# Kernel optimization log

Measured on AMD Instinct MI355X. Metric: run time of the kernel, lower is better.

The kernel has to match this reference:

```python
import jax, jax.numpy as jnp
import numpy as np

C = 32          # mid_channel / in_channel
B = 8           # batch size (number of scenes)
N = 2_000_000   # total points across batch
BN_EPS = 1e-4   # BatchNorm1d eps from norm_fn


def setup_inputs() -> dict:
    key = jax.random.key(0)
    ks = jax.random.split(key, 8)
    s = 0.05
    return {
        "feats": jax.random.normal(ks[0], (N, C), dtype=jnp.float32),
        "batch_idxs": jnp.sort(jax.random.randint(ks[1], (N,), 0, B, dtype=jnp.int32)),
        "off_w1": jax.random.normal(ks[2], (C, C), dtype=jnp.float32) * s,
        "off_b1": jnp.zeros((C,), jnp.float32),
        "bn_gamma": jnp.ones((C,), jnp.float32),   # set_bn_init fills 1.0
        "bn_beta": jnp.zeros((C,), jnp.float32),   # set_bn_init fills 0.0
        "off_w2": jax.random.normal(ks[3], (C, 3), dtype=jnp.float32) * s,
        "off_b2": jnp.zeros((3,), jnp.float32),
        "mask_w1": jax.random.normal(ks[4], (C, C), dtype=jnp.float32) * s,
        "mask_b1": jnp.zeros((C,), jnp.float32),
        "mask_w2": jax.random.normal(ks[5], (C, 1), dtype=jnp.float32) * s,
        "mask_b2": jnp.zeros((1,), jnp.float32),
        "iou_w": jax.random.normal(ks[6], (C, 1), dtype=jnp.float32) * s,
        "iou_b": jnp.zeros((1,), jnp.float32),
    }


def reference(feats, batch_idxs, off_w1, off_b1, bn_gamma, bn_beta, off_w2, off_b2,
              mask_w1, mask_b1, mask_w2, mask_b2, iou_w, iou_b):
    # offset_linear = MLP([C, C, 3], norm_fn=BatchNorm1d): Linear -> BN -> ReLU -> Linear
    h = feats @ off_w1 + off_b1                      # [N, C]
    mu = h.mean(axis=0)
    var = jnp.mean(jnp.square(h - mu), axis=0)       # biased var (torch BN training fwd)
    h = (h - mu) * jax.lax.rsqrt(var + BN_EPS) * bn_gamma + bn_beta
    h = jax.nn.relu(h)
    pt_offsets = h @ off_w2 + off_b2                 # [N, 3]

    # mask_linear = MLP([C, C, 1], norm_fn=None): Linear -> ReLU -> Linear
    m = jax.nn.relu(feats @ mask_w1 + mask_b1)       # [N, C]
    mask_scores = m @ mask_w2 + mask_b2              # [N, 1]

    # global_pool: scatter mean of features over per-batch segments (batch offsets)
    ones = jnp.ones((feats.shape[0],), feats.dtype)
    counts = jax.ops.segment_sum(ones, batch_idxs, num_segments=B)          # [B]
    pooled = jax.ops.segment_sum(feats, batch_idxs, num_segments=B)         # [B, C]
    pooled = pooled / jnp.maximum(counts, 1.0)[:, None]

    # iou_score_linear on the pooled proposal feature
    iou_scores = pooled @ iou_w + iou_b              # [B, 1]
    return pt_offsets, mask_scores, pooled, iou_scores
```

## Files before the change

kernel.cpp:

```cpp
#include <hip/hip_runtime.h>

#define TPB 256
#define GRID1 1024
#define GRID2 1024
#define MSLICES 8

typedef __attribute__((ext_vector_type(8))) short short8;
typedef __attribute__((ext_vector_type(4))) float floatx4;

__device__ __forceinline__ unsigned short bf_trunc(float f){
    union { float f; unsigned u; } c; c.f = f;
    return (unsigned short)(c.u >> 16);
}
__device__ __forceinline__ unsigned short bf_rne(float f){
    union { float f; unsigned u; } c; c.f = f;
    unsigned r = c.u + 0x7fffu + ((c.u >> 16) & 1u);
    return (unsigned short)(r >> 16);
}
__device__ __forceinline__ unsigned pack_bf(float lo, float hi){
    union { float f; unsigned u; } a, b; a.f = lo; b.f = hi;
    return __builtin_amdgcn_perm(b.u, a.u, 0x07060302u);
}
__device__ __forceinline__ float bfbits(unsigned short u){
    union { unsigned u; float f; } c; c.u = ((unsigned)u) << 16; return c.f;
}

__global__ void lb_kernel(const int* __restrict__ bidx, int* __restrict__ ws_lb,
                          int N, int B)
{
    const int t = threadIdx.x;
    if (t <= B){
        int lo = 0, hi = N;
        while (lo < hi){
            const int mid = (lo + hi) >> 1;
            if (bidx[mid] < t) lo = mid + 1; else hi = mid;
        }
        ws_lb[t] = lo;
    }
}

__global__ __launch_bounds__(TPB) void pass1_kernel(
    const float* __restrict__ feats, const int* __restrict__ ws_lb,
    float* __restrict__ ws_pool, float* __restrict__ ws_M,
    int N, int B)
{
    __shared__ float s_stage[TPB/64][1024];
    __shared__ float s_pool[8][32];
    __shared__ float s_M[3][256];
    __shared__ int   s_lb[9];

    const int tid  = threadIdx.x;
    const int lane = tid & 63;
    const int wv   = tid >> 6;
    const int p = lane & 15;
    const int q = lane >> 4;

    ((float*)s_pool)[tid] = 0.f;
    for (int i = tid; i < 768; i += TPB) ((float*)s_M)[i] = 0.f;
    if (tid <= B) s_lb[tid] = ws_lb[tid];
    __syncthreads();

    float pacc[4] = {0,0,0,0};
    floatx4 acc00 = {0,0,0,0}, acc01 = {0,0,0,0}, acc11 = {0,0,0,0};

    const int ngroups = (N + 31) >> 5;
    const int nw  = gridDim.x * (TPB / 64);
    const int wid = blockIdx.x * (TPB / 64) + wv;
    const int g0  = (int)((long)wid       * ngroups / nw);
    const int gE  = (int)((long)(wid + 1) * ngroups / nw);

    int curb = 0;
    { const int r = g0 << 5; while (curb < B - 1 && r >= s_lb[curb + 1]) curb++; }
    int lbn = s_lb[curb + 1];

    float* sw = &s_stage[wv][0];
    const int wrow  = lane >> 3;
    const int wg    = (lane & 7) ^ wrow;
    const int cbase = (lane & 7) << 2;
    const int wo0 = ( 0 + wrow) * 32 + (wg << 2);
    const int wo1 = ( 8 + wrow) * 32 + (wg << 2);
    const int wo2 = (16 + wrow) * 32 + (wg << 2);
    const int wo3 = (24 + wrow) * 32 + (wg << 2);

    floatx4 sv0 = {0,0,0,0}, sv1 = {0,0,0,0}, sv2 = {0,0,0,0}, sv3 = {0,0,0,0};
    if (g0 < gE){
        const float* gp = feats + ((size_t)g0 << 10) + (lane << 2);
        const int r = (g0 << 5) + wrow;
        if (r + 24 < N){
            sv0 = *(const floatx4*)(gp);
            sv1 = *(const floatx4*)(gp + 256);
            sv2 = *(const floatx4*)(gp + 512);
            sv3 = *(const floatx4*)(gp + 768);
        } else {
            if (r      < N) sv0 = *(const floatx4*)(gp);
            if (r +  8 < N) sv1 = *(const floatx4*)(gp + 256);
            if (r + 16 < N) sv2 = *(const floatx4*)(gp + 512);
            if (r + 24 < N) sv3 = *(const floatx4*)(gp + 768);
        }
    }

    for (int g = g0; g < gE; ++g){
        *(floatx4*)(sw + wo0) = sv0;
        *(floatx4*)(sw + wo1) = sv1;
        *(floatx4*)(sw + wo2) = sv2;
        *(floatx4*)(sw + wo3) = sv3;

        floatx4 nv0 = {0,0,0,0}, nv1 = {0,0,0,0}, nv2 = {0,0,0,0}, nv3 = {0,0,0,0};
        if (g + 1 < gE){
            const float* gp = feats + ((size_t)(g + 1) << 10) + (lane << 2);
            const int r = ((g + 1) << 5) + wrow;
            if (r + 24 < N){
                nv0 = *(const floatx4*)(gp);
                nv1 = *(const floatx4*)(gp + 256);
                nv2 = *(const floatx4*)(gp + 512);
                nv3 = *(const floatx4*)(gp + 768);
            } else {
                if (r      < N) nv0 = *(const floatx4*)(gp);
                if (r +  8 < N) nv1 = *(const floatx4*)(gp + 256);
                if (r + 16 < N) nv2 = *(const floatx4*)(gp + 512);
                if (r + 24 < N) nv3 = *(const floatx4*)(gp + 768);
            }
        }

        const int r0 = g << 5;
        if (r0 >= lbn){
#pragma unroll
            for (int j = 0; j < 4; ++j){
                if (pacc[j] != 0.f) atomicAdd(&s_pool[curb][cbase + j], pacc[j]);
                pacc[j] = 0.f;
            }
            do { curb++; } while (curb < B - 1 && r0 >= s_lb[curb + 1]);
            lbn = s_lb[curb + 1];
        }
        const bool slow = (r0 + 31 >= lbn) || (r0 + 31 >= N);

        if (!slow){
            pacc[0] += sv0[0] + sv1[0] + sv2[0] + sv3[0];
            pacc[1] += sv0[1] + sv1[1] + sv2[1] + sv3[1];
            pacc[2] += sv0[2] + sv1[2] + sv2[2] + sv3[2];
            pacc[3] += sv0[3] + sv1[3] + sv2[3] + sv3[3];
        } else {
#define SLOWROW(SV, L) { \
            const int row = r0 + (L * 8) + wrow; \
            if (row < N){ \
                int bl = curb; \
                for (int c = curb + 1; c < B; ++c) bl += (row >= s_lb[c]); \
                atomicAdd(&s_pool[bl][cbase + 0], SV[0]); \
                atomicAdd(&s_pool[bl][cbase + 1], SV[1]); \
                atomicAdd(&s_pool[bl][cbase + 2], SV[2]); \
                atomicAdd(&s_pool[bl][cbase + 3], SV[3]); \
            } }
            SLOWROW(sv0, 0) SLOWROW(sv1, 1) SLOWROW(sv2, 2) SLOWROW(sv3, 3)
#undef SLOWROW
        }

        short8 hi0, lo0, hi1, lo1;
#pragma unroll
        for (int j = 0; j < 8; ++j){
            const int row = q * 8 + j;
            const int e2  = row & 7;
            {
                const int c = p;
                const float v = sw[row * 32 + ((((c >> 2) ^ e2) << 2) + (c & 3))];
                const unsigned short hb = bf_trunc(v);
                hi0[j] = (short)hb;
                lo0[j] = (short)bf_trunc(v - bfbits(hb));
            }
            {
                const int c = 16 + p;
                const float v = sw[row * 32 + ((((c >> 2) ^ e2) << 2) + (c & 3))];
                const unsigned short hb = bf_trunc(v);
                hi1[j] = (short)hb;
                lo1[j] = (short)bf_trunc(v - bfbits(hb));
            }
        }

        acc00 = __builtin_amdgcn_mfma_f32_16x16x32_bf16(hi0, hi0, acc00, 0, 0, 0);
        acc00 = __builtin_amdgcn_mfma_f32_16x16x32_bf16(hi0, lo0, acc00, 0, 0, 0);
        acc00 = __builtin_amdgcn_mfma_f32_16x16x32_bf16(lo0, hi0, acc00, 0, 0, 0);
        acc01 = __builtin_amdgcn_mfma_f32_16x16x32_bf16(hi0, hi1, acc01, 0, 0, 0);
        acc01 = __builtin_amdgcn_mfma_f32_16x16x32_bf16(hi0, lo1, acc01, 0, 0, 0);
        acc01 = __builtin_amdgcn_mfma_f32_16x16x32_bf16(lo0, hi1, acc01, 0, 0, 0);
        acc11 = __builtin_amdgcn_mfma_f32_16x16x32_bf16(hi1, hi1, acc11, 0, 0, 0);
        acc11 = __builtin_amdgcn_mfma_f32_16x16x32_bf16(hi1, lo1, acc11, 0, 0, 0);
        acc11 = __builtin_amdgcn_mfma_f32_16x16x32_bf16(lo1, hi1, acc11, 0, 0, 0);

        sv0 = nv0; sv1 = nv1; sv2 = nv2; sv3 = nv3;
    }

#pragma unroll
    for (int j = 0; j < 4; ++j){
        if (pacc[j] != 0.f) atomicAdd(&s_pool[curb][cbase + j], pacc[j]);
    }
#pragma unroll
    for (int r = 0; r < 4; ++r){
        const int idx = (4 * q + r) * 16 + p;
        atomicAdd(&s_M[0][idx], acc00[r]);
        atomicAdd(&s_M[1][idx], acc01[r]);
        atomicAdd(&s_M[2][idx], acc11[r]);
    }
    __syncthreads();
    {
        const float pv = ((float*)s_pool)[tid];
        if (pv != 0.f) atomicAdd(&ws_pool[tid], pv);
    }
    {
        float* slice = ws_M + (size_t)(blockIdx.x % MSLICES) * 768;
        for (int i = tid; i < 768; i += TPB){
            const float v = ((float*)s_M)[i];
            if (v != 0.f) atomicAdd(slice + i, v);
        }
    }
}

__global__ __launch_bounds__(TPB) void pass2_kernel(
    const float* __restrict__ feats, const int* __restrict__ ws_lb,
    const float* __restrict__ w1,
    const float* __restrict__ gamma, const float* __restrict__ beta,
    const float* __restrict__ w2, const float* __restrict__ b2,
    const float* __restrict__ mw1, const float* __restrict__ mb1,
    const float* __restrict__ mw2, const float* __restrict__ mb2,
    const float* __restrict__ iw, const float* __restrict__ ib,
    const float* __restrict__ ws_pool, const float* __restrict__ ws_M,
    float* __restrict__ pt_out, float* __restrict__ mask_out,
    float* __restrict__ pooled_out, float* __restrict__ iou_out,
    int N, int B)
{
    __shared__ float s_stage[TPB/64][1024];
    __shared__ float s_w[1024];
    __shared__ float s_M2[1024];
    __shared__ float s_mu[32];
    __shared__ float s_var[32];
    __shared__ float s_sc[32];
    __shared__ float s_bp[32];
    __shared__ float s_pooled[256];
    __shared__ int   s_lb[9];

    const int tid  = threadIdx.x;
    const int lane = tid & 63;
    const int wv   = tid >> 6;
    const int p = lane & 15;
    const int q = lane >> 4;

    for (int i = tid; i < 1024; i += TPB) s_w[i] = w1[i];
    for (int i = tid; i < 256; i += TPB){
        float v0 = 0.f, v1 = 0.f, v2 = 0.f;
#pragma unroll
        for (int s = 0; s < MSLICES; ++s){
            v0 += ws_M[(size_t)s * 768 + i];
            v1 += ws_M[(size_t)s * 768 + 256 + i];
            v2 += ws_M[(size_t)s * 768 + 512 + i];
        }
        const int m = i >> 4, n = i & 15;
        s_M2[m * 32 + n] = v0;
        s_M2[(16 + m) * 32 + 16 + n] = v2;
        s_M2[m * 32 + 16 + n] = v1;
        s_M2[(16 + n) * 32 + m] = v1;
    }
    if (tid < 32){
        float s = 0.f;
        for (int b = 0; b < B; ++b) s += ws_pool[b * 32 + tid];
        s_mu[tid]  = s / (float)N;
        s_var[tid] = 0.f;
    }
    if (tid <= B) s_lb[tid] = ws_lb[tid];
    __syncthreads();

    {
        const int c = tid & 31, a0 = (tid >> 5) * 4;
        float part = 0.f;
#pragma unroll
        for (int a = a0; a < a0 + 4; ++a){
            float t2 = 0.f;
#pragma unroll
            for (int b = 0; b < 32; ++b) t2 = fmaf(s_w[b * 32 + c], s_M2[a * 32 + b], t2);
            part = fmaf(s_w[a * 32 + c], t2, part);
        }
        atomicAdd(&s_var[c], part);
    }
    __syncthreads();
    if (tid < 32){
        float muh = 0.f;
#pragma unroll
        for (int a = 0; a < 32; ++a) muh = fmaf(s_mu[a], s_w[a * 32 + tid], muh);
        const float var = s_var[tid] / (float)N - muh * muh;
        const float s   = gamma[tid] * rsqrtf(var + 1e-4f);
        s_sc[tid] = s;
        s_bp[tid] = beta[tid] - muh * s;
    }
    __syncthreads();

    if (blockIdx.x == 0){
        if (tid < B * 32){
            const int bb = tid >> 5;
            const float cnt = fmaxf((float)(s_lb[bb + 1] - s_lb[bb]), 1.f);
            const float pv = ws_pool[tid] / cnt;
            s_pooled[tid]   = pv;
            pooled_out[tid] = pv;
        }
        __syncthreads();
        if (tid < B){
            float acc = ib[0];
#pragma unroll
            for (int i = 0; i < 32; ++i) acc = fmaf(s_pooled[tid * 32 + i], iw[i], acc);
            iou_out[tid] = acc;
        }
    }

    short8 aw0, aw1, am0, am1;
    floatx4 ci_h0, ci_h1, ci_m0, ci_m1;
    float mw2v[8], w2v[24];
    const float sc0 = s_sc[p], sc1 = s_sc[16 + p];
#pragma unroll
    for (int j = 0; j < 8; ++j){
        const int k = q * 8 + j;
        aw0[j] = (short)bf_rne(s_w[k * 32 + p]      * sc0);
        aw1[j] = (short)bf_rne(s_w[k * 32 + 16 + p] * sc1);
        am0[j] = (short)bf_rne(mw1[k * 32 + p]);
        am1[j] = (short)bf_rne(mw1[k * 32 + 16 + p]);
    }
#pragma unroll
    for (int r = 0; r < 4; ++r){
        const int c0 = q * 4 + r, c1 = 16 + q * 4 + r;
        ci_h0[r] = s_bp[c0];  ci_h1[r] = s_bp[c1];
        ci_m0[r] = mb1[c0];   ci_m1[r] = mb1[c1];
        mw2v[r] = mw2[c0];    mw2v[4 + r] = mw2[c1];
    }
#pragma unroll
    for (int i = 0; i < 8; ++i){
        const int ch = (i >> 2) * 16 + q * 4 + (i & 3);
        w2v[i]      = w2[ch * 3 + 0];
        w2v[8 + i]  = w2[ch * 3 + 1];
        w2v[16 + i] = w2[ch * 3 + 2];
    }
    const float b2v0 = b2[0], b2v1 = b2[1], b2v2 = b2[2];
    const float mb2s = mb2[0];

    const int ngroups = (N + 31) >> 5;
    const int nw  = gridDim.x * (TPB / 64);
    const int wid = blockIdx.x * (TPB / 64) + wv;
    const int g0  = (int)((long)wid       * ngroups / nw);
    const int gE  = (int)((long)(wid + 1) * ngroups / nw);

    float* sw = &s_stage[wv][0];
    const int wrow = lane >> 3;
    const int wg   = (lane & 7) ^ wrow;
    const int wo0 = ( 0 + wrow) * 32 + (wg << 2);
    const int wo1 = ( 8 + wrow) * 32 + (wg << 2);
    const int wo2 = (16 + wrow) * 32 + (wg << 2);
    const int wo3 = (24 + wrow) * 32 + (wg << 2);
    const int e = p & 7;
    const int ra0 = p * 32        + ((((q << 1)    ) ^ e) << 2);
    const int ra1 = p * 32        + ((((q << 1) + 1) ^ e) << 2);
    const int rb0 = (16 + p) * 32 + ((((q << 1)    ) ^ e) << 2);
    const int rb1 = (16 + p) * 32 + ((((q << 1) + 1) ^ e) << 2);

    floatx4 sv0 = {0,0,0,0}, sv1 = {0,0,0,0}, sv2 = {0,0,0,0}, sv3 = {0,0,0,0};
    if (g0 < gE){
        const float* gp = feats + ((size_t)g0 << 10) + (lane << 2);
        const int r = (g0 << 5) + wrow;
        if (r + 24 < N){
            sv0 = *(const floatx4*)(gp);
            sv1 = *(const floatx4*)(gp + 256);
            sv2 = *(const floatx4*)(gp + 512);
            sv3 = *(const floatx4*)(gp + 768);
        } else {
            if (r      < N) sv0 = *(const floatx4*)(gp);
            if (r +  8 < N) sv1 = *(const floatx4*)(gp + 256);
            if (r + 16 < N) sv2 = *(const floatx4*)(gp + 512);
            if (r + 24 < N) sv3 = *(const floatx4*)(gp + 768);
        }
    }

    for (int g = g0; g < gE; ++g){
        *(floatx4*)(sw + wo0) = sv0;
        *(floatx4*)(sw + wo1) = sv1;
        *(floatx4*)(sw + wo2) = sv2;
        *(floatx4*)(sw + wo3) = sv3;

        floatx4 nv0 = {0,0,0,0}, nv1 = {0,0,0,0}, nv2 = {0,0,0,0}, nv3 = {0,0,0,0};
        if (g + 1 < gE){
            const float* gp = feats + ((size_t)(g + 1) << 10) + (lane << 2);
            const int r = ((g + 1) << 5) + wrow;
            if (r + 24 < N){
                nv0 = *(const floatx4*)(gp);
                nv1 = *(const floatx4*)(gp + 256);
                nv2 = *(const floatx4*)(gp + 512);
                nv3 = *(const floatx4*)(gp + 768);
            } else {
                if (r      < N) nv0 = *(const floatx4*)(gp);
                if (r +  8 < N) nv1 = *(const floatx4*)(gp + 256);
                if (r + 16 < N) nv2 = *(const floatx4*)(gp + 512);
                if (r + 24 < N) nv3 = *(const floatx4*)(gp + 768);
            }
        }

        const floatx4 vA0 = *(const floatx4*)(sw + ra0);
        const floatx4 vA1 = *(const floatx4*)(sw + ra1);
        const floatx4 vB0 = *(const floatx4*)(sw + rb0);
        const floatx4 vB1 = *(const floatx4*)(sw + rb1);

        short8 bfA, bfB;
        {
            unsigned* ba = (unsigned*)&bfA;
            ba[0] = pack_bf(vA0[0], vA0[1]); ba[1] = pack_bf(vA0[2], vA0[3]);
            ba[2] = pack_bf(vA1[0], vA1[1]); ba[3] = pack_bf(vA1[2], vA1[3]);
            unsigned* bb = (unsigned*)&bfB;
            bb[0] = pack_bf(vB0[0], vB0[1]); bb[1] = pack_bf(vB0[2], vB0[3]);
            bb[2] = pack_bf(vB1[0], vB1[1]); bb[3] = pack_bf(vB1[2], vB1[3]);
        }

        const floatx4 cA0 = __builtin_amdgcn_mfma_f32_16x16x32_bf16(aw0, bfA, ci_h0, 0, 0, 0);
        const floatx4 cA1 = __builtin_amdgcn_mfma_f32_16x16x32_bf16(aw1, bfA, ci_h1, 0, 0, 0);
        const floatx4 mA0 = __builtin_amdgcn_mfma_f32_16x16x32_bf16(am0, bfA, ci_m0, 0, 0, 0);
        const floatx4 mA1 = __builtin_amdgcn_mfma_f32_16x16x32_bf16(am1, bfA, ci_m1, 0, 0, 0);
        const floatx4 cB0 = __builtin_amdgcn_mfma_f32_16x16x32_bf16(aw0, bfB, ci_h0, 0, 0, 0);
        const floatx4 cB1 = __builtin_amdgcn_mfma_f32_16x16x32_bf16(aw1, bfB, ci_h1, 0, 0, 0);
        const floatx4 mB0 = __builtin_amdgcn_mfma_f32_16x16x32_bf16(am0, bfB, ci_m0, 0, 0, 0);
        const floatx4 mB1 = __builtin_amdgcn_mfma_f32_16x16x32_bf16(am1, bfB, ci_m1, 0, 0, 0);

        float sA0 = 0.f, sA1 = 0.f, sA2 = 0.f, sB0 = 0.f, sB1 = 0.f, sB2 = 0.f;
        float tmA = 0.f, tmB = 0.f;
#pragma unroll
        for (int r = 0; r < 4; ++r){
            const float a0 = fmaxf(cA0[r], 0.f);
            const float a1 = fmaxf(cA1[r], 0.f);
            sA0 = fmaf(a0, w2v[r],      sA0); sA0 = fmaf(a1, w2v[4 + r],  sA0);
            sA1 = fmaf(a0, w2v[8 + r],  sA1); sA1 = fmaf(a1, w2v[12 + r], sA1);
            sA2 = fmaf(a0, w2v[16 + r], sA2); sA2 = fmaf(a1, w2v[20 + r], sA2);
            const float b0 = fmaxf(cB0[r], 0.f);
            const float b1v = fmaxf(cB1[r], 0.f);
            sB0 = fmaf(b0, w2v[r],      sB0); sB0 = fmaf(b1v, w2v[4 + r],  sB0);
            sB1 = fmaf(b0, w2v[8 + r],  sB1); sB1 = fmaf(b1v, w2v[12 + r], sB1);
            sB2 = fmaf(b0, w2v[16 + r], sB2); sB2 = fmaf(b1v, w2v[20 + r], sB2);
            tmA = fmaf(fmaxf(mA0[r], 0.f), mw2v[r],     tmA);
            tmA = fmaf(fmaxf(mA1[r], 0.f), mw2v[4 + r], tmA);
            tmB = fmaf(fmaxf(mB0[r], 0.f), mw2v[r],     tmB);
            tmB = fmaf(fmaxf(mB1[r], 0.f), mw2v[4 + r], tmB);
        }
        sA0 += __shfl_xor(sA0, 16, 64); sA0 += __shfl_xor(sA0, 32, 64);
        sA1 += __shfl_xor(sA1, 16, 64); sA1 += __shfl_xor(sA1, 32, 64);
        sA2 += __shfl_xor(sA2, 16, 64); sA2 += __shfl_xor(sA2, 32, 64);
        sB0 += __shfl_xor(sB0, 16, 64); sB0 += __shfl_xor(sB0, 32, 64);
        sB1 += __shfl_xor(sB1, 16, 64); sB1 += __shfl_xor(sB1, 32, 64);
        sB2 += __shfl_xor(sB2, 16, 64); sB2 += __shfl_xor(sB2, 32, 64);
        tmA += __shfl_xor(tmA, 16, 64); tmA += __shfl_xor(tmA, 32, 64);
        tmB += __shfl_xor(tmB, 16, 64); tmB += __shfl_xor(tmB, 32, 64);

        const int r0 = g << 5;
        const int rA = r0 + p, rB = r0 + 16 + p;
        if (lane < 48 && rA < N){
            const float val = (q == 0) ? (sA0 + b2v0) : ((q == 1) ? (sA1 + b2v1) : (sA2 + b2v2));
            pt_out[(size_t)rA * 3 + q] = val;
        }
        if (lane < 48 && rB < N){
            const float val = (q == 0) ? (sB0 + b2v0) : ((q == 1) ? (sB1 + b2v1) : (sB2 + b2v2));
            pt_out[(size_t)rB * 3 + q] = val;
        }
        if (q == 0 && rA < N) mask_out[rA] = tmA + mb2s;
        if (q == 0 && rB < N) mask_out[rB] = tmB + mb2s;

        sv0 = nv0; sv1 = nv1; sv2 = nv2; sv3 = nv3;
    }
}

extern "C" void kernel_launch(void* const* d_in, const int* in_sizes, int n_in,
                              void* d_out, int out_size, void* d_ws, size_t ws_size,
                              hipStream_t stream) {
    const float* feats = (const float*)d_in[0];
    const int*   bidx  = (const int*)d_in[1];
    const float* w1    = (const float*)d_in[2];
    const float* b1    = (const float*)d_in[3];
    const float* gamma = (const float*)d_in[4];
    const float* beta  = (const float*)d_in[5];
    const float* w2    = (const float*)d_in[6];
    const float* b2    = (const float*)d_in[7];
    const float* mw1   = (const float*)d_in[8];
    const float* mb1   = (const float*)d_in[9];
    const float* mw2   = (const float*)d_in[10];
    const float* mb2   = (const float*)d_in[11];
    const float* iw    = (const float*)d_in[12];
    const float* ib    = (const float*)d_in[13];
    (void)b1;

    const int N = in_sizes[0] / 32;
    const int B = (out_size - 4 * N) / 33;

    float* out    = (float*)d_out;
    float* pt     = out;
    float* mask   = out + (size_t)3 * N;
    float* pooled = out + (size_t)4 * N;
    float* iou    = pooled + (size_t)B * 32;

    float* ws      = (float*)d_ws;
    float* ws_pool = ws;
    float* ws_M    = ws + 256;
    int*   ws_lb   = (int*)(ws + 256 + MSLICES * 768);

    (void)hipMemsetAsync(ws, 0, (size_t)(256 + MSLICES * 768) * sizeof(float), stream);

    lb_kernel<<<1, 64, 0, stream>>>(bidx, ws_lb, N, B);
    pass1_kernel<<<GRID1, TPB, 0, stream>>>(feats, ws_lb, ws_pool, ws_M, N, B);
    pass2_kernel<<<GRID2, TPB, 0, stream>>>(feats, ws_lb, w1, gamma, beta, w2, b2,
                                            mw1, mb1, mw2, mb2, iw, ib,
                                            ws_pool, ws_M,
                                            pt, mask, pooled, iou, N, B);
}
```

Measured before the change: 470.0 us.

## Fuse both passes into one persistent kernel with grid barrier and reverse traversal

```diff
diff --git a/kernel.cpp b/kernel.cpp
--- a/kernel.cpp
+++ b/kernel.cpp
@@ -1,8 +1,6 @@
 #include <hip/hip_runtime.h>
 
 #define TPB 256
-#define GRID1 1024
-#define GRID2 1024
 #define MSLICES 8
 
 typedef __attribute__((ext_vector_type(8))) short short8;
@@ -39,14 +37,29 @@
     }
 }
 
-__global__ __launch_bounds__(TPB) void pass1_kernel(
+__global__ __launch_bounds__(TPB, 3) void fused_kernel(
     const float* __restrict__ feats, const int* __restrict__ ws_lb,
+    const float* __restrict__ w1,
+    const float* __restrict__ gamma, const float* __restrict__ beta,
+    const float* __restrict__ w2, const float* __restrict__ b2,
+    const float* __restrict__ mw1, const float* __restrict__ mb1,
+    const float* __restrict__ mw2, const float* __restrict__ mb2,
+    const float* __restrict__ iw, const float* __restrict__ ib,
     float* __restrict__ ws_pool, float* __restrict__ ws_M,
+    unsigned* __restrict__ ws_cnt,
+    float* __restrict__ pt_out, float* __restrict__ mask_out,
+    float* __restrict__ pooled_out, float* __restrict__ iou_out,
     int N, int B)
 {
     __shared__ float s_stage[TPB/64][1024];
     __shared__ float s_pool[8][32];
     __shared__ float s_M[3][256];
+    __shared__ float s_w[1024];
+    __shared__ float s_M2[1024];
+    __shared__ float s_mu[32];
+    __shared__ float s_var[32];
+    __shared__ float s_sc[32];
+    __shared__ float s_bp[32];
     __shared__ int   s_lb[9];
 
     const int tid  = threadIdx.x;
@@ -211,45 +224,24 @@
             if (v != 0.f) atomicAdd(slice + i, v);
         }
     }
-}
-
-__global__ __launch_bounds__(TPB) void pass2_kernel(
-    const float* __restrict__ feats, const int* __restrict__ ws_lb,
-    const float* __restrict__ w1,
-    const float* __restrict__ gamma, const float* __restrict__ beta,
-    const float* __restrict__ w2, const float* __restrict__ b2,
-    const float* __restrict__ mw1, const float* __restrict__ mb1,
-    const float* __restrict__ mw2, const float* __restrict__ mb2,
-    const float* __restrict__ iw, const float* __restrict__ ib,
-    const float* __restrict__ ws_pool, const float* __restrict__ ws_M,
-    float* __restrict__ pt_out, float* __restrict__ mask_out,
-    float* __restrict__ pooled_out, float* __restrict__ iou_out,
-    int N, int B)
-{
-    __shared__ float s_stage[TPB/64][1024];
-    __shared__ float s_w[1024];
-    __shared__ float s_M2[1024];
-    __shared__ float s_mu[32];
-    __shared__ float s_var[32];
-    __shared__ float s_sc[32];
-    __shared__ float s_bp[32];
-    __shared__ float s_pooled[256];
-    __shared__ int   s_lb[9];
-
-    const int tid  = threadIdx.x;
-    const int lane = tid & 63;
-    const int wv   = tid >> 6;
-    const int p = lane & 15;
-    const int q = lane >> 4;
+
+    __syncthreads();
+    if (tid == 0){
+        __hip_atomic_fetch_add(ws_cnt, 1u, __ATOMIC_ACQ_REL, __HIP_MEMORY_SCOPE_AGENT);
+        const unsigned nb = gridDim.x;
+        while (__hip_atomic_load(ws_cnt, __ATOMIC_ACQUIRE, __HIP_MEMORY_SCOPE_AGENT) < nb)
+            __builtin_amdgcn_s_sleep(16);
+    }
+    __syncthreads();
 
     for (int i = tid; i < 1024; i += TPB) s_w[i] = w1[i];
     for (int i = tid; i < 256; i += TPB){
         float v0 = 0.f, v1 = 0.f, v2 = 0.f;
 #pragma unroll
         for (int s = 0; s < MSLICES; ++s){
-            v0 += ws_M[(size_t)s * 768 + i];
-            v1 += ws_M[(size_t)s * 768 + 256 + i];
-            v2 += ws_M[(size_t)s * 768 + 512 + i];
+            v0 += __hip_atomic_load(&ws_M[(size_t)s * 768 + i],       __ATOMIC_RELAXED, __HIP_MEMORY_SCOPE_AGENT);
+            v1 += __hip_atomic_load(&ws_M[(size_t)s * 768 + 256 + i], __ATOMIC_RELAXED, __HIP_MEMORY_SCOPE_AGENT);
+            v2 += __hip_atomic_load(&ws_M[(size_t)s * 768 + 512 + i], __ATOMIC_RELAXED, __HIP_MEMORY_SCOPE_AGENT);
         }
         const int m = i >> 4, n = i & 15;
         s_M2[m * 32 + n] = v0;
@@ -259,13 +251,12 @@
     }
     if (tid < 32){
         float s = 0.f;
-        for (int b = 0; b < B; ++b) s += ws_pool[b * 32 + tid];
+        for (int b = 0; b < B; ++b)
+            s += __hip_atomic_load(&ws_pool[b * 32 + tid], __ATOMIC_RELAXED, __HIP_MEMORY_SCOPE_AGENT);
         s_mu[tid]  = s / (float)N;
         s_var[tid] = 0.f;
     }
-    if (tid <= B) s_lb[tid] = ws_lb[tid];
-    __syncthreads();
-
+    __syncthreads();
     {
         const int c = tid & 31, a0 = (tid >> 5) * 4;
         float part = 0.f;
@@ -291,10 +282,11 @@
     __syncthreads();
 
     if (blockIdx.x == 0){
+        __shared__ float s_pooled[256];
         if (tid < B * 32){
             const int bb = tid >> 5;
             const float cnt = fmaxf((float)(s_lb[bb + 1] - s_lb[bb]), 1.f);
-            const float pv = ws_pool[tid] / cnt;
+            const float pv = __hip_atomic_load(&ws_pool[tid], __ATOMIC_RELAXED, __HIP_MEMORY_SCOPE_AGENT) / cnt;
             s_pooled[tid]   = pv;
             pooled_out[tid] = pv;
         }
@@ -336,52 +328,40 @@
     const float b2v0 = b2[0], b2v1 = b2[1], b2v2 = b2[2];
     const float mb2s = mb2[0];
 
-    const int ngroups = (N + 31) >> 5;
-    const int nw  = gridDim.x * (TPB / 64);
-    const int wid = blockIdx.x * (TPB / 64) + wv;
-    const int g0  = (int)((long)wid       * ngroups / nw);
-    const int gE  = (int)((long)(wid + 1) * ngroups / nw);
-
-    float* sw = &s_stage[wv][0];
-    const int wrow = lane >> 3;
-    const int wg   = (lane & 7) ^ wrow;
-    const int wo0 = ( 0 + wrow) * 32 + (wg << 2);
-    const int wo1 = ( 8 + wrow) * 32 + (wg << 2);
-    const int wo2 = (16 + wrow) * 32 + (wg << 2);
-    const int wo3 = (24 + wrow) * 32 + (wg << 2);
     const int e = p & 7;
     const int ra0 = p * 32        + ((((q << 1)    ) ^ e) << 2);
     const int ra1 = p * 32        + ((((q << 1) + 1) ^ e) << 2);
     const int rb0 = (16 + p) * 32 + ((((q << 1)    ) ^ e) << 2);
     const int rb1 = (16 + p) * 32 + ((((q << 1) + 1) ^ e) << 2);
 
-    floatx4 sv0 = {0,0,0,0}, sv1 = {0,0,0,0}, sv2 = {0,0,0,0}, sv3 = {0,0,0,0};
+    floatx4 rv0 = {0,0,0,0}, rv1 = {0,0,0,0}, rv2 = {0,0,0,0}, rv3 = {0,0,0,0};
     if (g0 < gE){
-        const float* gp = feats + ((size_t)g0 << 10) + (lane << 2);
-        const int r = (g0 << 5) + wrow;
+        const int gs = gE - 1;
+        const float* gp = feats + ((size_t)gs << 10) + (lane << 2);
+        const int r = (gs << 5) + wrow;
         if (r + 24 < N){
-            sv0 = *(const floatx4*)(gp);
-            sv1 = *(const floatx4*)(gp + 256);
-            sv2 = *(const floatx4*)(gp + 512);
-            sv3 = *(const floatx4*)(gp + 768);
+            rv0 = *(const floatx4*)(gp);
+            rv1 = *(const floatx4*)(gp + 256);
+            rv2 = *(const floatx4*)(gp + 512);
+            rv3 = *(const floatx4*)(gp + 768);
         } else {
-            if (r      < N) sv0 = *(const floatx4*)(gp);
-            if (r +  8 < N) sv1 = *(const floatx4*)(gp + 256);
-            if (r + 16 < N) sv2 = *(const floatx4*)(gp + 512);
-            if (r + 24 < N) sv3 = *(const floatx4*)(gp + 768);
-        }
-    }
-
-    for (int g = g0; g < gE; ++g){
-        *(floatx4*)(sw + wo0) = sv0;
-        *(floatx4*)(sw + wo1) = sv1;
-        *(floatx4*)(sw + wo2) = sv2;
-        *(floatx4*)(sw + wo3) = sv3;
+            if (r      < N) rv0 = *(const floatx4*)(gp);
+            if (r +  8 < N) rv1 = *(const floatx4*)(gp + 256);
+            if (r + 16 < N) rv2 = *(const floatx4*)(gp + 512);
+            if (r + 24 < N) rv3 = *(const floatx4*)(gp + 768);
+        }
+    }
+
+    for (int g = gE - 1; g >= g0; --g){
+        *(floatx4*)(sw + wo0) = rv0;
+        *(floatx4*)(sw + wo1) = rv1;
+        *(floatx4*)(sw + wo2) = rv2;
+        *(floatx4*)(sw + wo3) = rv3;
 
         floatx4 nv0 = {0,0,0,0}, nv1 = {0,0,0,0}, nv2 = {0,0,0,0}, nv3 = {0,0,0,0};
-        if (g + 1 < gE){
-            const float* gp = feats + ((size_t)(g + 1) << 10) + (lane << 2);
-            const int r = ((g + 1) << 5) + wrow;
+        if (g - 1 >= g0){
+            const float* gp = feats + ((size_t)(g - 1) << 10) + (lane << 2);
+            const int r = ((g - 1) << 5) + wrow;
             if (r + 24 < N){
                 nv0 = *(const floatx4*)(gp);
                 nv1 = *(const floatx4*)(gp + 256);
@@ -460,7 +440,7 @@
         if (q == 0 && rA < N) mask_out[rA] = tmA + mb2s;
         if (q == 0 && rB < N) mask_out[rB] = tmB + mb2s;
 
-        sv0 = nv0; sv1 = nv1; sv2 = nv2; sv3 = nv3;
+        rv0 = nv0; rv1 = nv1; rv2 = nv2; rv3 = nv3;
     }
 }
 
@@ -492,17 +472,23 @@
     float* pooled = out + (size_t)4 * N;
     float* iou    = pooled + (size_t)B * 32;
 
-    float* ws      = (float*)d_ws;
-    float* ws_pool = ws;
-    float* ws_M    = ws + 256;
-    int*   ws_lb   = (int*)(ws + 256 + MSLICES * 768);
-
-    (void)hipMemsetAsync(ws, 0, (size_t)(256 + MSLICES * 768) * sizeof(float), stream);
+    float*    ws      = (float*)d_ws;
+    float*    ws_pool = ws;
+    float*    ws_M    = ws + 256;
+    unsigned* ws_cnt  = (unsigned*)(ws + 256 + MSLICES * 768);
+    int*      ws_lb   = (int*)(ws + 256 + MSLICES * 768 + 16);
+
+    (void)hipMemsetAsync(ws, 0, (size_t)(256 + MSLICES * 768 + 16) * sizeof(float), stream);
+
+    int per = 0;
+    (void)hipOccupancyMaxActiveBlocksPerMultiprocessor(&per, fused_kernel, TPB, 0);
+    int grid = per * 256;
+    if (grid > 768) grid = 768;
+    if (grid < 64)  grid = 64;
 
     lb_kernel<<<1, 64, 0, stream>>>(bidx, ws_lb, N, B);
-    pass1_kernel<<<GRID1, TPB, 0, stream>>>(feats, ws_lb, ws_pool, ws_M, N, B);
-    pass2_kernel<<<GRID2, TPB, 0, stream>>>(feats, ws_lb, w1, gamma, beta, w2, b2,
-                                            mw1, mb1, mw2, mb2, iw, ib,
-                                            ws_pool, ws_M,
-                                            pt, mask, pooled, iou, N, B);
-}
+    fused_kernel<<<grid, TPB, 0, stream>>>(feats, ws_lb, w1, gamma, beta, w2, b2,
+                                           mw1, mb1, mw2, mb2, iw, ib,
+                                           ws_pool, ws_M, ws_cnt,
+                                           pt, mask, pooled, iou, N, B);
+}
```

New measurement: 480.8 us. 2.3% more time.
